# Optimization experiments

Hardware: AMD Instinct MI355X
Metric: run time of the kernel (lower is better)

The kernel has to match this reference:

```python
import jax, jax.numpy as jnp
import numpy as np

WS = 8      # window size
NH = 8      # num heads
ED = 256    # embed dim
HD = ED // NH  # head dim


def conv2d(x, w, b):
    # x: [B,C,H,W], w: [O,I,3,3] (torch OIHW), SAME padding, stride 1
    y = jax.lax.conv_general_dilated(x, w, (1, 1), 'SAME',
                                     dimension_numbers=('NCHW', 'OIHW', 'NCHW'))
    return y + b[None, :, None, None]


def linear(x, w, b):
    # torch Linear: y = x @ W^T + b, w: [out,in]
    return jnp.einsum('bnc,oc->bno', x, w) + b


def window_partition(x, ws):
    B, C, H, W = x.shape
    x = x.reshape(B, C, H // ws, ws, W // ws, ws)
    x = jnp.transpose(x, (0, 2, 4, 3, 5, 1))  # B, H/ws, W/ws, ws, ws, C
    return x.reshape(-1, ws * ws, C)


def window_reverse(win, H, W, ws, C):
    nW = (H // ws) * (W // ws)
    B = win.shape[0] // nW
    x = win.reshape(B, H // ws, W // ws, ws, ws, C)
    x = jnp.transpose(x, (0, 5, 1, 3, 2, 4))
    return x.reshape(B, C, H, W)


def setup_inputs() -> dict:
    key = jax.random.key(0)
    ks = jax.random.split(key, 24)
    s = 0.02
    inp = {
        'xmap': jax.random.normal(ks[0], (4, ED, 256, 256), jnp.float32),
        'xfeat': jax.random.normal(ks[1], (4, 32, 256, 256), jnp.float32),
        'cmap_w': jax.random.normal(ks[2], (ED, ED, 3, 3), jnp.float32) * s,
        'cmap_b': jnp.zeros((ED,), jnp.float32),
        'cfeat_w': jax.random.normal(ks[3], (ED, 32, 3, 3), jnp.float32) * s,
        'cfeat_b': jnp.zeros((ED,), jnp.float32),
        'qxmap_w': jax.random.normal(ks[4], (ED, ED), jnp.float32) * s,
        'qxmap_b': jnp.zeros((ED,), jnp.float32),
        'kxmap_w': jax.random.normal(ks[5], (ED, ED), jnp.float32) * s,
        'kxmap_b': jnp.zeros((ED,), jnp.float32),
        'vxmap_w': jax.random.normal(ks[6], (ED, ED), jnp.float32) * s,
        'vxmap_b': jnp.zeros((ED,), jnp.float32),
        'qxfeat_w': jax.random.normal(ks[7], (ED, ED), jnp.float32) * s,
        'qxfeat_b': jnp.zeros((ED,), jnp.float32),
        'kxfeat_w': jax.random.normal(ks[8], (ED, ED), jnp.float32) * s,
        'kxfeat_b': jnp.zeros((ED,), jnp.float32),
        'proj_w': jax.random.normal(ks[9], (ED, ED), jnp.float32) * s,
        'proj_b': jnp.zeros((ED,), jnp.float32),
        'cout_w': jax.random.normal(ks[10], (ED, ED, 3, 3), jnp.float32) * s,
        'cout_b': jnp.zeros((ED,), jnp.float32),
    }
    return inp


def reference(xmap, xfeat, cmap_w, cmap_b, cfeat_w, cfeat_b,
              qxmap_w, qxmap_b, kxmap_w, kxmap_b, vxmap_w, vxmap_b,
              qxfeat_w, qxfeat_b, kxfeat_w, kxfeat_b,
              proj_w, proj_b, cout_w, cout_b):
    B, C, H, W = xmap.shape  # xfeat matches spatial size -> no interpolate branch
    xmap = conv2d(xmap, cmap_w, cmap_b)
    identity = xmap
    wm = window_partition(xmap, WS)                        # [Bw, N, C]
    wf = window_partition(conv2d(xfeat, cfeat_w, cfeat_b), WS)
    Bw, N, _ = wm.shape

    def heads(t):
        return jnp.transpose(t.reshape(Bw, N, NH, HD), (0, 2, 1, 3))  # [Bw,H,N,D]

    q_m = heads(linear(wm, qxmap_w, qxmap_b))
    k_m = heads(linear(wm, kxmap_w, kxmap_b))
    v_m = heads(linear(wm, vxmap_w, vxmap_b))
    q_f = heads(linear(wf, qxfeat_w, qxfeat_b))
    k_f = heads(linear(wf, kxfeat_w, kxfeat_b))

    q_g = jax.nn.sigmoid(q_f) * q_m
    k_g = jax.nn.sigmoid(k_f) * k_m

    scale = 1.0 / jnp.sqrt(jnp.asarray(HD, q_g.dtype))
    attn = jax.nn.softmax(jnp.einsum('bhnd,bhmd->bhnm', q_g, k_g) * scale, axis=-1)
    out = jnp.einsum('bhnm,bhmd->bhnd', attn, v_m)         # [Bw,H,N,D]
    out = jnp.transpose(out, (0, 2, 1, 3)).reshape(Bw, N, C)
    out = window_reverse(linear(out, proj_w, proj_b), H, W, WS, C)
    return conv2d(out, cout_w, cout_b) + identity
```

## Files before the change

### kernel.cpp

```cpp
#include <hip/hip_runtime.h>
#include <hip/hip_bf16.h>
#include <cstdint>
#include <math.h>

using bf16 = __hip_bfloat16;
typedef __attribute__((ext_vector_type(4))) float f32x4;
typedef __attribute__((ext_vector_type(8))) short s16x8;
typedef __attribute__((ext_vector_type(4))) short s16x4;

#define AS3(p) ((__attribute__((address_space(3))) void *)(p))
#define AS1(p) ((const __attribute__((address_space(1))) void *)(p))

static constexpr int Himg = 256, Wimg = 256, Bimg = 4;
static constexpr int HWimg = Himg * Wimg;
static constexpr int Ttok = Bimg * HWimg;

__device__ __forceinline__ void gld16(bf16* lds, const bf16* g) {
  __builtin_amdgcn_global_load_lds(AS1(g), AS3(lds), 16, 0, 0);
}

__device__ __forceinline__ unsigned short f2u(float f) {
  bf16 b = __float2bfloat16(f);
  unsigned short u; __builtin_memcpy(&u, &b, 2); return u;
}

__device__ __forceinline__ int remap_lin(int bid, int total) {
  return (bid & 7) * (total >> 3) + (bid >> 3);
}
__device__ __forceinline__ void remap_tile(int bid, int total, int NY, int BMv, int& t0, int& n0) {
  int lin = remap_lin(bid, total);
  t0 = (lin / NY) * BMv;
  n0 = (lin % NY) * 128;
}

__global__ void k_zero4k(float* p) {
  p[blockIdx.x * 256 + threadIdx.x] = 0.f;
}

__global__ void k_castf2b(const float* __restrict__ s, bf16* __restrict__ d, int n) {
  int i = blockIdx.x * 256 + threadIdx.x;
  if (i < n) d[i] = __float2bfloat16(s[i]);
}

__global__ void k_copyf(const float* __restrict__ s, float* __restrict__ d, int n) {
  int i = blockIdx.x * 256 + threadIdx.x;
  if (i < n) d[i] = s[i];
}

__global__ void k_permconv(const float* __restrict__ w, bf16* __restrict__ o, int I) {
  int idx = blockIdx.x * 256 + threadIdx.x;
  int tot = 256 * 9 * I;
  if (idx >= tot) return;
  int i   = idx % I;
  int rem = idx / I;
  int tap = rem % 9;
  int oc  = rem / 9;
  o[idx] = __float2bfloat16(w[(oc * I + i) * 9 + tap]);
}

__global__ void k_tohwc(const float* __restrict__ src, bf16* __restrict__ dst, int C) {
  int bh = blockIdx.x;
  int w0 = blockIdx.y * 32;
  int c0 = blockIdx.z * 32;
  int b = bh / Himg, h = bh % Himg;
  __shared__ float tile[32][33];
  int tid = threadIdx.x;
  int x = tid & 31, y = tid >> 5;
  const float* sp = src + (size_t)b * C * HWimg + (size_t)h * Wimg;
#pragma unroll
  for (int p = 0; p < 4; ++p) {
    int cl = y + p * 8;
    tile[cl][x] = sp[(size_t)(c0 + cl) * HWimg + w0 + x];
  }
  __syncthreads();
#pragma unroll
  for (int p = 0; p < 4; ++p) {
    int wl = y + p * 8;
    dst[((size_t)bh * Wimg + w0 + wl) * C + c0 + x] = __float2bfloat16(tile[x][wl]);
  }
}

template <int CIN, int TAPS, int EPI>
__global__ void __launch_bounds__(512, 1)
k_gemm8(const bf16* __restrict__ Ain, const bf16* __restrict__ BT,
        const float* __restrict__ bias,
        bf16* __restrict__ outb, int ldo, float* __restrict__ outf,
        const bf16* __restrict__ ident,
        const bf16* __restrict__ zp)
{
  constexpr int KTOT = TAPS * CIN;
  const int t0 = remap_lin(blockIdx.x, gridDim.x) * 256;
  const int tid  = threadIdx.x;
  const int wave = tid >> 6, lane = tid & 63;
  const int wr = wave >> 2, wc = wave & 3;
  const int fr = lane & 15, fq = lane >> 4;

  __shared__ __attribute__((aligned(16))) char arena[132608];
  bf16* A0k0 = (bf16*)(arena);
  bf16* A0k1 = (bf16*)(arena + 16384);
  bf16* A1k0 = (bf16*)(arena + 32768);
  bf16* A1k1 = (bf16*)(arena + 49152);
  bf16* B0k0 = (bf16*)(arena + 65536);
  bf16* B0k1 = (bf16*)(arena + 81920);
  bf16* B1k0 = (bf16*)(arena + 98304);
  bf16* B1k1 = (bf16*)(arena + 114688);

  f32x4 acc[8][4] = {};
  s16x8 bfr[4];

  const int slot8 = (fq ^ ((fr >> 1) & 3)) * 8;
  const int aoff  = (wr * 128 + fr) * 32 + slot8;
  const int boff  = (wc * 64 + fr) * 32 + slot8;
  const int ldsl  = (tid & 3) * 8;
  const int scol  = ((tid & 3) ^ ((tid >> 3) & 3)) * 8;
  const int srow  = tid >> 2;

  const bf16* Bb0 = BT + (size_t)srow * KTOT + scol;
  const bf16* Bb1 = BT + (size_t)(128 + srow) * KTOT + scol;
  const bf16* Aa0 = Ain + (size_t)(t0 + srow) * CIN + scol;
  const bf16* Aa1 = Ain + (size_t)(t0 + 128 + srow) * CIN + scol;
  const bf16 *a0c = Aa0, *a1c = Aa1, *a0n = Aa0, *a1n = Aa1;
  const int hU = (t0 >> 8) & 255;

  auto mkbase = [&](int tap, const bf16*& o0, const bf16*& o1) {
    const int dy = tap / 3 - 1, dx = tap % 3 - 1;
    const bool rowok = ((unsigned)(hU + dy)) < 256u;
    const long gb = (long)t0 + dy * Wimg + dx;
    o0 = (rowok && (unsigned)(srow + dx) < 256u)
             ? Ain + (gb + srow) * CIN + scol : zp + scol;
    o1 = (rowok && (unsigned)(128 + srow + dx) < 256u)
             ? Ain + (gb + 128 + srow) * CIN + scol : zp + scol;
  };

#define STA8(DST, P0, P1, CE) do {                                              \
    gld16(DST + srow * 32 + ldsl, (P0) + (CE));                                 \
    gld16(DST + (128 + srow) * 32 + ldsl, (P1) + (CE));                         \
  } while (0)
#define STB8(DST, KE) do {                                                      \
    gld16(DST + srow * 32 + ldsl, Bb0 + (KE));                                  \
    gld16(DST + (128 + srow) * 32 + ldsl, Bb1 + (KE));                          \
  } while (0)

#define NVMs
#define VM4 asm volatile("s_waitcnt vmcnt(4)" ::: "memory")
#define VM0 asm volatile("s_waitcnt vmcnt(0)" ::: "memory")

#define PHO(RA, RB, MH, READB, ...) do {                                         \
    s16x8 af_[4];                                                                \
    _Pragma("unroll") for (int q_ = 0; q_ < 4; ++q_)                             \
      af_[q_] = *(const s16x8*)((RA) + aoff + ((MH) * 4 + q_) * 512);            \
    if (READB) {                                                                 \
      _Pragma("unroll") for (int n_ = 0; n_ < 4; ++n_)                           \
        bfr[n_] = *(const s16x8*)((RB) + boff + n_ * 512);                       \
    }                                                                            \
    __VA_ARGS__;                                                                 \
    asm volatile("s_waitcnt lgkmcnt(0)" ::: "memory");                           \
    __builtin_amdgcn_sched_barrier(0);                                           \
    __builtin_amdgcn_s_setprio(1);                                               \
    _Pragma("unroll") for (int q_ = 0; q_ < 4; ++q_)                             \
      _Pragma("unroll") for (int n_ = 0; n_ < 4; ++n_)                           \
        acc[(MH) * 4 + q_][n_] = __builtin_amdgcn_mfma_f32_16x16x32_bf16(        \
            af_[q_], bfr[n_], acc[(MH) * 4 + q_][n_], 0, 0, 0);                  \
    __builtin_amdgcn_s_setprio(0);                                               \
  } while (0)

#define PHE(RA, RB, MH, READB, VMSTMT, ...) do {                                 \
    s16x8 af_[4];                                                                \
    _Pragma("unroll") for (int q_ = 0; q_ < 4; ++q_)                             \
      af_[q_] = *(const s16x8*)((RA) + aoff + ((MH) * 4 + q_) * 512);            \
    if (READB) {                                                                 \
      _Pragma("unroll") for (int n_ = 0; n_ < 4; ++n_)                           \
        bfr[n_] = *(const s16x8*)((RB) + boff + n_ * 512);                       \
    }                                                                            \
    __VA_ARGS__;                                                                 \
    VMSTMT;                                                                      \
    __builtin_amdgcn_sched_barrier(0);                                           \
    __builtin_amdgcn_s_barrier();                                                \
    asm volatile("s_waitcnt lgkmcnt(0)" ::: "memory");                           \
    __builtin_amdgcn_sched_barrier(0);                                           \
    __builtin_amdgcn_s_setprio(1);                                               \
    _Pragma("unroll") for (int q_ = 0; q_ < 4; ++q_)                             \
      _Pragma("unroll") for (int n_ = 0; n_ < 4; ++n_)                           \
        acc[(MH) * 4 + q_][n_] = __builtin_amdgcn_mfma_f32_16x16x32_bf16(        \
            af_[q_], bfr[n_], acc[(MH) * 4 + q_][n_], 0, 0, 0);                  \
    __builtin_amdgcn_s_setprio(0);                                               \
  } while (0)

  if constexpr (TAPS == 9 && CIN == 256) {
    mkbase(0, a0c, a1c);
    mkbase(1, a0n, a1n);
    STA8(A0k0, a0c, a1c, 0);  STB8(B0k0, 0);
    STA8(A0k1, a0c, a1c, 32); STB8(B0k1, 32);
    VM4;
    __builtin_amdgcn_s_barrier();
#pragma unroll 1
    for (int tap = 0; tap < 8; ++tap) {
      PHO(A0k0, B0k0, 0, 1, STA8(A1k0, a0c, a1c, 64));
      PHE(A0k0, B0k0, 1, 0, VM4, STB8(B1k0, 64));
      PHO(A0k1, B0k1, 0, 1, STA8(A1k1, a0c, a1c, 96));
      PHE(A0k1, B0k1, 1, 0, VM4, STB8(B1k1, 96));
      PHO(A1k0, B1k0, 0, 1, STA8(A0k0, a0c, a1c, 128));
      PHE(A1k0, B1k0, 1, 0, VM4, STB8(B0k0, 128));
      PHO(A1k1, B1k1, 0, 1, STA8(A0k1, a0c, a1c, 160));
      PHE(A1k1, B1k1, 1, 0, VM4, STB8(B0k1, 160));
      PHO(A0k0, B0k0, 0, 1, STA8(A1k0, a0c, a1c, 192));
      PHE(A0k0, B0k0, 1, 0, VM4, STB8(B1k0, 192));
      PHO(A0k1, B0k1, 0, 1, STA8(A1k1, a0c, a1c, 224));
      PHE(A0k1, B0k1, 1, 0, VM4, STB8(B1k1, 224));
      PHO(A1k0, B1k0, 0, 1, STA8(A0k0, a0n, a1n, 0));
      PHE(A1k0, B1k0, 1, 0, VM4, STB8(B0k0, 256));
      PHO(A1k1, B1k1, 0, 1, STA8(A0k1, a0n, a1n, 32));
      PHE(A1k1, B1k1, 1, 0, VM4, STB8(B0k1, 288));
      a0c = a0n; a1c = a1n;
      if (tap + 2 < 9) mkbase(tap + 2, a0n, a1n);
      Bb0 += 256; Bb1 += 256;
    }
    PHO(A0k0, B0k0, 0, 1, STA8(A1k0, a0c, a1c, 64));
    PHE(A0k0, B0k0, 1, 0, VM4, STB8(B1k0, 64));
    PHO(A0k1, B0k1, 0, 1, STA8(A1k1, a0c, a1c, 96));
    PHE(A0k1, B0k1, 1, 0, VM4, STB8(B1k1, 96));
    PHO(A1k0, B1k0, 0, 1, STA8(A0k0, a0c, a1c, 128));
    PHE(A1k0, B1k0, 1, 0, VM4, STB8(B0k0, 128));
    PHO(A1k1, B1k1, 0, 1, STA8(A0k1, a0c, a1c, 160));
    PHE(A1k1, B1k1, 1, 0, VM4, STB8(B0k1, 160));
    PHO(A0k0, B0k0, 0, 1, STA8(A1k0, a0c, a1c, 192));
    PHE(A0k0, B0k0, 1, 0, VM4, STB8(B1k0, 192));
    PHO(A0k1, B0k1, 0, 1, STA8(A1k1, a0c, a1c, 224));
    PHE(A0k1, B0k1, 1, 0, VM4, STB8(B1k1, 224));
    PHO(A1k0, B1k0, 0, 1, );
    PHE(A1k0, B1k0, 1, 0, VM0, );
    PHO(A1k1, B1k1, 0, 1, );
    PHE(A1k1, B1k1, 1, 0, NVMs, );
  } else if constexpr (TAPS == 9) {
    mkbase(0, a0c, a1c);
    STA8(A0k0, a0c, a1c, 0);  STB8(B0k0, 0);
    mkbase(1, a0c, a1c);
    STA8(A0k1, a0c, a1c, 0);  STB8(B0k1, 32);
    VM4;
    __builtin_amdgcn_s_barrier();
    PHO(A0k0, B0k0, 0, 1, mkbase(2, a0c, a1c); STA8(A1k0, a0c, a1c, 0));
    PHE(A0k0, B0k0, 1, 0, VM4, STB8(B1k0, 64));
    PHO(A0k1, B0k1, 0, 1, mkbase(3, a0c, a1c); STA8(A1k1, a0c, a1c, 0));
    PHE(A0k1, B0k1, 1, 0, VM4, STB8(B1k1, 96));
    PHO(A1k0, B1k0, 0, 1, mkbase(4, a0c, a1c); STA8(A0k0, a0c, a1c, 0));
    PHE(A1k0, B1k0, 1, 0, VM4, STB8(B0k0, 128));
    PHO(A1k1, B1k1, 0, 1, mkbase(5, a0c, a1c); STA8(A0k1, a0c, a1c, 0));
    PHE(A1k1, B1k1, 1, 0, VM4, STB8(B0k1, 160));
    PHO(A0k0, B0k0, 0, 1, mkbase(6, a0c, a1c); STA8(A1k0, a0c, a1c, 0));
    PHE(A0k0, B0k0, 1, 0, VM4, STB8(B1k0, 192));
    PHO(A0k1, B0k1, 0, 1, mkbase(7, a0c, a1c); STA8(A1k1, a0c, a1c, 0));
    PHE(A0k1, B0k1, 1, 0, VM4, STB8(B1k1, 224));
    PHO(A1k0, B1k0, 0, 1, mkbase(8, a0c, a1c); STA8(A0k0, a0c, a1c, 0));
    PHE(A1k0, B1k0, 1, 0, VM4, STB8(B0k0, 256));
    PHO(A1k1, B1k1, 0, 1, );
    PHE(A1k1, B1k1, 1, 0, VM0, );
    PHO(A0k0, B0k0, 0, 1, );
    PHE(A0k0, B0k0, 1, 0, NVMs, );
  } else {
    STA8(A0k0, Aa0, Aa1, 0);  STB8(B0k0, 0);
    STA8(A0k1, Aa0, Aa1, 32); STB8(B0k1, 32);
    VM4;
    __builtin_amdgcn_s_barrier();
    PHO(A0k0, B0k0, 0, 1, STA8(A1k0, Aa0, Aa1, 64));
    PHE(A0k0, B0k0, 1, 0, VM4, STB8(B1k0, 64));
    PHO(A0k1, B0k1, 0, 1, STA8(A1k1, Aa0, Aa1, 96));
    PHE(A0k1, B0k1, 1, 0, VM4, STB8(B1k1, 96));
    PHO(A1k0, B1k0, 0, 1, STA8(A0k0, Aa0, Aa1, 128));
    PHE(A1k0, B1k0, 1, 0, VM4, STB8(B0k0, 128));
    PHO(A1k1, B1k1, 0, 1, STA8(A0k1, Aa0, Aa1, 160));
    PHE(A1k1, B1k1, 1, 0, VM4, STB8(B0k1, 160));
    PHO(A0k0, B0k0, 0, 1, STA8(A1k0, Aa0, Aa1, 192));
    PHE(A0k0, B0k0, 1, 0, VM4, STB8(B1k0, 192));
    PHO(A0k1, B0k1, 0, 1, STA8(A1k1, Aa0, Aa1, 224));
    PHE(A0k1, B0k1, 1, 0, VM4, STB8(B1k1, 224));
    PHO(A1k0, B1k0, 0, 1, );
    PHE(A1k0, B1k0, 1, 0, VM0, );
    PHO(A1k1, B1k1, 0, 1, );
    PHE(A1k1, B1k1, 1, 0, NVMs, );
  }
#undef PHO
#undef PHE
#undef STA8
#undef STB8
#undef NVMs
#undef VM4
#undef VM0

  if (EPI == 2) {
    float* TR = (float*)arena;
    const int bN = t0 >> 16, hN = (t0 >> 8) & 255;
#pragma unroll 1
    for (int chunk = 0; chunk < 2; ++chunk) {
      __builtin_amdgcn_s_barrier();
      if ((wc >> 1) == chunk) {
#pragma unroll
        for (int m = 0; m < 8; ++m)
#pragma unroll
          for (int n = 0; n < 4; ++n) {
            const int col = wc * 64 + n * 16 + fr;
            const int cl  = (wc & 1) * 64 + n * 16 + fr;
            const float bb = bias[col];
#pragma unroll
            for (int j = 0; j < 4; ++j) {
              const int row = wr * 128 + m * 16 + fq * 4 + j;
              const size_t t = (size_t)t0 + row;
              TR[cl * 259 + row] = acc[m][n][j] + bb +
                                   __bfloat162float(ident[t * 256 + col]);
            }
          }
      }
      __builtin_amdgcn_s_barrier();
      {
        const int cl = tid >> 2, wo = (tid & 3) * 4;
        const int c = chunk * 128 + cl;
        float* dp = outf + (((size_t)bN * 256 + c) * 256 + hN) * 256;
#pragma unroll
        for (int q = 0; q < 16; ++q)
          *(f32x4*)(dp + wo + q * 16) = *(const f32x4*)&TR[cl * 259 + wo + q * 16];
      }
    }
    return;
  }

#pragma unroll
  for (int m = 0; m < 8; ++m) {
#pragma unroll
    for (int n = 0; n < 4; ++n) {
      const int col = wc * 64 + n * 16 + fr;
#pragma unroll
      for (int j = 0; j < 4; ++j) {
        const int row = wr * 128 + m * 16 + fq * 4 + j;
        const size_t t = (size_t)t0 + row;
        outb[t * ldo + col] = __float2bfloat16(acc[m][n][j] + bias[col]);
      }
    }
  }
}

__global__ void __launch_bounds__(256, 2)
k_gemm_qkv(const bf16* __restrict__ Am, const bf16* __restrict__ Af,
           const bf16* __restrict__ Bm, const bf16* __restrict__ Bf,
           const float* __restrict__ bm, const float* __restrict__ bfi,
           bf16* __restrict__ out)
{
  int t0, n0;
  remap_tile(blockIdx.x, gridDim.x, 4, 128, t0, n0);
  const int tid = threadIdx.x;
  const int wave = tid >> 6, lane = tid & 63;
  const int seg = lane & 3;
  const int rr  = lane >> 2;

  __shared__ bf16 sA0[128 * 32];
  __shared__ bf16 sA1[128 * 32];
  __shared__ bf16 sA2[128 * 32];
  __shared__ bf16 sB0[128 * 32];
  __shared__ bf16 sB1[128 * 32];
  __shared__ bf16 sB2[128 * 32];

  f32x4 accm[4][4] = {};
  f32x4 accf[4][4] = {};

  const int wr = wave >> 1, wc = wave & 1;
  const int fr = lane & 15, fq = lane >> 4;
  const int sseg = (seg ^ ((rr >> 1) & 3)) * 8;
  const int slot = (fq ^ ((fr >> 1) & 3)) * 8;

#define STAGEQ(WA, WB, SV) do {                                                 \
    const int k0_ = ((SV) >> 1) * 32;                                           \
    const bf16* A_ = ((SV) & 1) ? Af : Am;                                      \
    const bf16* B_ = ((SV) & 1) ? Bf : Bm;                                      \
    _Pragma("unroll") for (int i_ = 0; i_ < 2; ++i_) {                          \
      const int r_ = wave * 32 + i_ * 16 + rr;                                  \
      gld16(WA + (wave * 32 + i_ * 16) * 32, A_ + (size_t)(t0 + r_) * 256 + k0_ + sseg); \
      gld16(WB + (wave * 32 + i_ * 16) * 32, B_ + (size_t)(n0 + r_) * 256 + k0_ + sseg); \
    }                                                                           \
  } while (0)

#define QSTEP(RA, RB, WA, WB, SV, LASTF) do {                                   \
    if (LASTF) { asm volatile("s_waitcnt vmcnt(0)" ::: "memory"); }             \
    else       { asm volatile("s_waitcnt vmcnt(4)" ::: "memory"); }             \
    __builtin_amdgcn_s_barrier();                                               \
    s16x8 af_[4], bf_[4];                                                       \
    _Pragma("unroll") for (int m_ = 0; m_ < 4; ++m_)                            \
      af_[m_] = *(const s16x8*)(RA + (wr * 64 + m_ * 16 + fr) * 32 + slot);     \
    _Pragma("unroll") for (int n_ = 0; n_ < 4; ++n_)                            \
      bf_[n_] = *(const s16x8*)(RB + (wc * 64 + n_ * 16 + fr) * 32 + slot);     \
    if ((SV) + 2 < 16) STAGEQ(WA, WB, (SV) + 2);                                \
    __builtin_amdgcn_s_setprio(1);                                              \
    if ((SV) & 1) {                                                             \
      _Pragma("unroll") for (int m_ = 0; m_ < 4; ++m_)                          \
        _Pragma("unroll") for (int n_ = 0; n_ < 4; ++n_)                        \
          accf[m_][n_] = __builtin_amdgcn_mfma_f32_16x16x32_bf16(af_[m_], bf_[n_], accf[m_][n_], 0, 0, 0); \
    } else {                                                                    \
      _Pragma("unroll") for (int m_ = 0; m_ < 4; ++m_)                          \
        _Pragma("unroll") for (int n_ = 0; n_ < 4; ++n_)                        \
          accm[m_][n_] = __builtin_amdgcn_mfma_f32_16x16x32_bf16(af_[m_], bf_[n_], accm[m_][n_], 0, 0, 0); \
    }                                                                           \
    __builtin_amdgcn_s_setprio(0);                                              \
  } while (0)

  STAGEQ(sA0, sB0, 0);
  STAGEQ(sA1, sB1, 1);

  int s = 0;
#pragma unroll 1
  for (; s < 15; s += 3) {
    QSTEP(sA0, sB0, sA2, sB2, s,     false);
    QSTEP(sA1, sB1, sA0, sB0, s + 1, false);
    QSTEP(sA2, sB2, sA1, sB1, s + 2, false);
  }
  QSTEP(sA0, sB0, sA2, sB2, 15, true);
#undef QSTEP
#undef STAGEQ

#pragma unroll
  for (int m = 0; m < 4; ++m) {
#pragma unroll
    for (int n = 0; n < 4; ++n) {
      const int col = n0 + wc * 64 + n * 16 + fr;
#pragma unroll
      for (int j = 0; j < 4; ++j) {
        const int row = wr * 64 + m * 16 + fq * 4 + j;
        const size_t t = (size_t)t0 + row;
        float v = accm[m][n][j] + bm[col];
        const float g = accf[m][n][j] + bfi[col];
        v *= 1.f / (1.f + __expf(-g));
        out[t * 768 + col] = __float2bfloat16(v);
      }
    }
  }
}

__global__ void __launch_bounds__(256, 4)
k_attn_mfma(const bf16* __restrict__ qkv, bf16* __restrict__ out) {
  __shared__ short smem[4 * 7424];
  const int tid = threadIdx.x;
  const int wave = tid >> 6, lane = tid & 63;
  const int fr = lane & 15, fq = lane >> 4;
  const int wi = blockIdx.x >> 1;
  const int head = (blockIdx.x & 1) * 4 + wave;
  const int b = wi >> 10, rem = wi & 1023, wh = rem >> 5, ww = rem & 31;
  const size_t tbase = (size_t)b * HWimg + (size_t)(wh * 8) * Wimg + ww * 8;

  short* Qs = smem + wave * 7424;
  short* Ks = Qs + 2560;
  short* VT = Qs + 5120;
  short* P  = Qs;
  short* Ol = Qs;

  auto tok = [&](int i) -> size_t {
    return tbase + (size_t)(i >> 3) * Wimg + (i & 7);
  };

  {
    const bf16* tb = qkv + tok(lane) * 768 + head * 32;
#pragma unroll
    for (int c = 0; c < 4; ++c) {
      s16x8 qv = *(const s16x8*)(tb + c * 8);
      s16x8 kv = *(const s16x8*)(tb + 256 + c * 8);
      s16x8 vv = *(const s16x8*)(tb + 512 + c * 8);
      *(s16x8*)(Qs + lane * 40 + c * 8) = qv;
      *(s16x8*)(Ks + lane * 40 + c * 8) = kv;
#pragma unroll
      for (int e = 0; e < 8; ++e) VT[(c * 8 + e) * 72 + lane] = vv[e];
    }
  }

  s16x8 kf[4], qf[4];
#pragma unroll
  for (int m = 0; m < 4; ++m)
    kf[m] = *(const s16x8*)(Ks + (fr + 16 * m) * 40 + fq * 8);
#pragma unroll
  for (int n = 0; n < 4; ++n)
    qf[n] = *(const s16x8*)(Qs + (fr + 16 * n) * 40 + fq * 8);

  f32x4 st[4][4] = {};
#pragma unroll
  for (int m = 0; m < 4; ++m)
#pragma unroll
    for (int n = 0; n < 4; ++n)
      st[m][n] = __builtin_amdgcn_mfma_f32_16x16x32_bf16(kf[m], qf[n], st[m][n], 0, 0, 0);

  const float scale = 0.17677669529663688f;
  float invs[4];
#pragma unroll
  for (int n = 0; n < 4; ++n) {
    float mx = -1e30f;
#pragma unroll
    for (int m = 0; m < 4; ++m)
#pragma unroll
      for (int j = 0; j < 4; ++j) mx = fmaxf(mx, st[m][n][j]);
    mx = fmaxf(mx, __shfl_xor(mx, 16));
    mx = fmaxf(mx, __shfl_xor(mx, 32));
    float sum = 0.f;
#pragma unroll
    for (int m = 0; m < 4; ++m) {
      s16x4 pk;
#pragma unroll
      for (int j = 0; j < 4; ++j) {
        float e = __expf((st[m][n][j] - mx) * scale);
        sum += e;
        pk[j] = (short)f2u(e);
      }
      *(s16x4*)(P + (fr + 16 * n) * 72 + 16 * m + 4 * fq) = pk;
    }
    sum += __shfl_xor(sum, 16);
    sum += __shfl_xor(sum, 32);
    invs[n] = 1.f / sum;
  }

  f32x4 oc[4][2] = {};
#pragma unroll
  for (int ks = 0; ks < 2; ++ks) {
    s16x8 pf[4], vf[2];
#pragma unroll
    for (int m = 0; m < 4; ++m)
      pf[m] = *(const s16x8*)(P + (fr + 16 * m) * 72 + ks * 32 + fq * 8);
#pragma unroll
    for (int n = 0; n < 2; ++n)
      vf[n] = *(const s16x8*)(VT + (fr + 16 * n) * 72 + ks * 32 + fq * 8);
#pragma unroll
    for (int m = 0; m < 4; ++m)
#pragma unroll
      for (int n = 0; n < 2; ++n)
        oc[m][n] = __builtin_amdgcn_mfma_f32_16x16x32_bf16(pf[m], vf[n], oc[m][n], 0, 0, 0);
  }

#pragma unroll
  for (int m = 0; m < 4; ++m)
#pragma unroll
    for (int j = 0; j < 4; ++j) {
      const float inv = __shfl(invs[m], 4 * fq + j);
      const int q = 16 * m + 4 * fq + j;
#pragma unroll
      for (int n = 0; n < 2; ++n)
        Ol[q * 40 + fr + 16 * n] = (short)f2u(oc[m][n][j] * inv);
    }
  {
    bf16* op = out + tok(lane) * 256 + head * 32;
#pragma unroll
    for (int c = 0; c < 4; ++c)
      *(s16x8*)(op + c * 8) = *(const s16x8*)(Ol + lane * 40 + c * 8);
  }
}

extern "C" void kernel_launch(void* const* d_in, const int* in_sizes, int n_in,
                              void* d_out, int out_size, void* d_ws, size_t ws_size,
                              hipStream_t stream) {
  const float* xmap    = (const float*)d_in[0];
  const float* xfeat   = (const float*)d_in[1];
  const float* cmap_w  = (const float*)d_in[2];
  const float* cmap_b  = (const float*)d_in[3];
  const float* cfeat_w = (const float*)d_in[4];
  const float* cfeat_b = (const float*)d_in[5];
  const float* qxmap_w = (const float*)d_in[6];
  const float* qxmap_b = (const float*)d_in[7];
  const float* kxmap_w = (const float*)d_in[8];
  const float* kxmap_b = (const float*)d_in[9];
  const float* vxmap_w = (const float*)d_in[10];
  const float* vxmap_b = (const float*)d_in[11];
  const float* qxfeat_w = (const float*)d_in[12];
  const float* qxfeat_b = (const float*)d_in[13];
  const float* kxfeat_w = (const float*)d_in[14];
  const float* kxfeat_b = (const float*)d_in[15];
  const float* proj_w  = (const float*)d_in[16];
  const float* proj_b  = (const float*)d_in[17];
  const float* cout_w  = (const float*)d_in[18];
  const float* cout_b  = (const float*)d_in[19];

  uint8_t* ws = (uint8_t*)d_ws;
  size_t off = 0;
  auto alloc = [&](size_t bytes) -> void* {
    void* p = ws + off;
    off += (bytes + 255) & ~(size_t)255;
    return p;
  };
  float* zp       = (float*)alloc(4096);
  bf16* cmap_wT   = (bf16*)alloc((size_t)2304 * 256 * 2);
  bf16* cout_wT   = (bf16*)alloc((size_t)2304 * 256 * 2);
  bf16* cfeat_wT  = (bf16*)alloc((size_t)288 * 256 * 2);
  bf16* lin_qkv_wT= (bf16*)alloc((size_t)768 * 256 * 2);
  bf16* lin_f_wT  = (bf16*)alloc((size_t)512 * 256 * 2);
  bf16* proj_wT   = (bf16*)alloc((size_t)256 * 256 * 2);
  float* bias_qkv = (float*)alloc(768 * 4);
  float* bias_f   = (float*)alloc(512 * 4);
  bf16* xm_nhwc   = (bf16*)alloc((size_t)Ttok * 256 * 2);
  bf16* xf_nhwc   = (bf16*)alloc((size_t)Ttok * 32 * 2);
  bf16* xc        = (bf16*)alloc((size_t)Ttok * 256 * 2);
  bf16* fc        = (bf16*)alloc((size_t)Ttok * 256 * 2);
  bf16* qkv       = (bf16*)alloc((size_t)Ttok * 768 * 2);
  bf16* attn_out  = xm_nhwc;
  bf16* proj_out  = fc;
  bf16* zpb = (bf16*)zp;

  k_zero4k<<<4, 256, 0, stream>>>(zp);
  k_permconv<<<(256 * 9 * 256 + 255) / 256, 256, 0, stream>>>(cmap_w, cmap_wT, 256);
  k_permconv<<<(256 * 9 * 256 + 255) / 256, 256, 0, stream>>>(cout_w, cout_wT, 256);
  k_permconv<<<(256 * 9 * 32 + 255) / 256, 256, 0, stream>>>(cfeat_w, cfeat_wT, 32);
  k_castf2b<<<256, 256, 0, stream>>>(qxmap_w, lin_qkv_wT, 65536);
  k_castf2b<<<256, 256, 0, stream>>>(kxmap_w, lin_qkv_wT + 65536, 65536);
  k_castf2b<<<256, 256, 0, stream>>>(vxmap_w, lin_qkv_wT + 131072, 65536);
  k_castf2b<<<256, 256, 0, stream>>>(qxfeat_w, lin_f_wT, 65536);
  k_castf2b<<<256, 256, 0, stream>>>(kxfeat_w, lin_f_wT + 65536, 65536);
  k_castf2b<<<256, 256, 0, stream>>>(proj_w, proj_wT, 65536);
  k_copyf<<<1, 256, 0, stream>>>(qxmap_b, bias_qkv, 256);
  k_copyf<<<1, 256, 0, stream>>>(kxmap_b, bias_qkv + 256, 256);
  k_copyf<<<1, 256, 0, stream>>>(vxmap_b, bias_qkv + 512, 256);
  k_copyf<<<1, 256, 0, stream>>>(qxfeat_b, bias_f, 256);
  k_copyf<<<1, 256, 0, stream>>>(kxfeat_b, bias_f + 256, 256);

  k_tohwc<<<dim3(Bimg * Himg, Wimg / 32, 256 / 32), 256, 0, stream>>>(xmap, xm_nhwc, 256);
  k_tohwc<<<dim3(Bimg * Himg, Wimg / 32, 1), 256, 0, stream>>>(xfeat, xf_nhwc, 32);

  const int NB = Ttok / 256;
  k_gemm8<256, 9, 0><<<dim3(NB), dim3(512), 0, stream>>>(
      xm_nhwc, cmap_wT, cmap_b, xc, 256, nullptr, nullptr, zpb);
  k_gemm8<32, 9, 0><<<dim3(NB), dim3(512), 0, stream>>>(
      xf_nhwc, cfeat_wT, cfeat_b, fc, 256, nullptr, nullptr, zpb);
  k_gemm8<256, 1, 0><<<dim3(NB), dim3(512), 0, stream>>>(
      xc, lin_qkv_wT + 131072, bias_qkv + 512, qkv + 512, 768, nullptr, nullptr, zpb);
  k_gemm_qkv<<<dim3((Ttok / 128) * 4), dim3(256), 0, stream>>>(
      xc, fc, lin_qkv_wT, lin_f_wT, bias_qkv, bias_f, qkv);
  k_attn_mfma<<<dim3(4096 * 2), dim3(256), 0, stream>>>(qkv, attn_out);
  k_gemm8<256, 1, 0><<<dim3(NB), dim3(512), 0, stream>>>(
      attn_out, proj_wT, proj_b, proj_out, 256, nullptr, nullptr, zpb);
  k_gemm8<256, 9, 2><<<dim3(NB), dim3(512), 0, stream>>>(
      proj_out, cout_wT, cout_b, nullptr, 0, (float*)d_out, xc, zpb);
}
```

Before: 1.392 ms.

## Restructure QKV gated GEMM into four-buffer half-step pipelined schedule

Replaces the three-buffer LDS ring in the fused QKV/gate GEMM with a four-buffer ring and a fully unrolled schedule. Each K-step is split into two half-phases, and A and B global-to-LDS loads are interleaved between the MFMA halves, with explicit lgkmcnt waits and sched_barriers. The aim is to overlap global loads with MFMA work more finely and to cut the number of block barriers per step. The cost is extra LDS (which may lower occupancy at two blocks per CU) and a hand-tuned ordering of vmcnt waits and barriers that must be exactly right to stay correct.

```diff
diff --git a/kernel.cpp b/kernel.cpp
--- a/kernel.cpp
+++ b/kernel.cpp
@@ -353,65 +353,116 @@
   __shared__ bf16 sA0[128 * 32];
   __shared__ bf16 sA1[128 * 32];
   __shared__ bf16 sA2[128 * 32];
+  __shared__ bf16 sA3[128 * 32];
   __shared__ bf16 sB0[128 * 32];
   __shared__ bf16 sB1[128 * 32];
   __shared__ bf16 sB2[128 * 32];
+  __shared__ bf16 sB3[128 * 32];
 
   f32x4 accm[4][4] = {};
   f32x4 accf[4][4] = {};
+  s16x8 bfr[4];
 
   const int wr = wave >> 1, wc = wave & 1;
   const int fr = lane & 15, fq = lane >> 4;
   const int sseg = (seg ^ ((rr >> 1) & 3)) * 8;
   const int slot = (fq ^ ((fr >> 1) & 3)) * 8;
 
-#define STAGEQ(WA, WB, SV) do {                                                 \
-    const int k0_ = ((SV) >> 1) * 32;                                           \
-    const bf16* A_ = ((SV) & 1) ? Af : Am;                                      \
-    const bf16* B_ = ((SV) & 1) ? Bf : Bm;                                      \
-    _Pragma("unroll") for (int i_ = 0; i_ < 2; ++i_) {                          \
-      const int r_ = wave * 32 + i_ * 16 + rr;                                  \
-      gld16(WA + (wave * 32 + i_ * 16) * 32, A_ + (size_t)(t0 + r_) * 256 + k0_ + sseg); \
-      gld16(WB + (wave * 32 + i_ * 16) * 32, B_ + (size_t)(n0 + r_) * 256 + k0_ + sseg); \
-    }                                                                           \
-  } while (0)
-
-#define QSTEP(RA, RB, WA, WB, SV, LASTF) do {                                   \
-    if (LASTF) { asm volatile("s_waitcnt vmcnt(0)" ::: "memory"); }             \
-    else       { asm volatile("s_waitcnt vmcnt(4)" ::: "memory"); }             \
+#define STQA(DST, AP, K0) do {                                                  \
+    _Pragma("unroll") for (int i_ = 0; i_ < 2; ++i_)                            \
+      gld16(DST + (wave * 32 + i_ * 16) * 32,                                   \
+            (AP) + (size_t)(t0 + wave * 32 + i_ * 16 + rr) * 256 + (K0) + sseg);\
+  } while (0)
+#define STQB(DST, BP, K0) do {                                                  \
+    _Pragma("unroll") for (int i_ = 0; i_ < 2; ++i_)                            \
+      gld16(DST + (wave * 32 + i_ * 16) * 32,                                   \
+            (BP) + (size_t)(n0 + wave * 32 + i_ * 16 + rr) * 256 + (K0) + sseg);\
+  } while (0)
+
+#define NVMs
+#define VM4 asm volatile("s_waitcnt vmcnt(4)" ::: "memory")
+#define VM0 asm volatile("s_waitcnt vmcnt(0)" ::: "memory")
+
+#define PHOQ(RA, RB, ACC, ...) do {                                             \
+    s16x8 af_[2];                                                               \
+    _Pragma("unroll") for (int m_ = 0; m_ < 2; ++m_)                            \
+      af_[m_] = *(const s16x8*)((RA) + (wr * 64 + m_ * 16 + fr) * 32 + slot);   \
+    _Pragma("unroll") for (int n_ = 0; n_ < 4; ++n_)                            \
+      bfr[n_] = *(const s16x8*)((RB) + (wc * 64 + n_ * 16 + fr) * 32 + slot);   \
+    __VA_ARGS__;                                                                \
+    asm volatile("s_waitcnt lgkmcnt(0)" ::: "memory");                          \
+    __builtin_amdgcn_sched_barrier(0);                                          \
+    __builtin_amdgcn_s_setprio(1);                                              \
+    _Pragma("unroll") for (int m_ = 0; m_ < 2; ++m_)                            \
+      _Pragma("unroll") for (int n_ = 0; n_ < 4; ++n_)                          \
+        ACC[m_][n_] = __builtin_amdgcn_mfma_f32_16x16x32_bf16(                  \
+            af_[m_], bfr[n_], ACC[m_][n_], 0, 0, 0);                            \
+    __builtin_amdgcn_s_setprio(0);                                              \
+  } while (0)
+
+#define PHEQ(RA, ACC, VMSTMT, ...) do {                                         \
+    s16x8 af_[2];                                                               \
+    _Pragma("unroll") for (int m_ = 0; m_ < 2; ++m_)                            \
+      af_[m_] = *(const s16x8*)((RA) + (wr * 64 + (2 + m_) * 16 + fr) * 32 + slot); \
+    __VA_ARGS__;                                                                \
+    VMSTMT;                                                                     \
+    __builtin_amdgcn_sched_barrier(0);                                          \
     __builtin_amdgcn_s_barrier();                                               \
-    s16x8 af_[4], bf_[4];                                                       \
-    _Pragma("unroll") for (int m_ = 0; m_ < 4; ++m_)                            \
-      af_[m_] = *(const s16x8*)(RA + (wr * 64 + m_ * 16 + fr) * 32 + slot);     \
-    _Pragma("unroll") for (int n_ = 0; n_ < 4; ++n_)                            \
-      bf_[n_] = *(const s16x8*)(RB + (wc * 64 + n_ * 16 + fr) * 32 + slot);     \
-    if ((SV) + 2 < 16) STAGEQ(WA, WB, (SV) + 2);                                \
+    asm volatile("s_waitcnt lgkmcnt(0)" ::: "memory");                          \
+    __builtin_amdgcn_sched_barrier(0);                                          \
     __builtin_amdgcn_s_setprio(1);                                              \
-    if ((SV) & 1) {                                                             \
-      _Pragma("unroll") for (int m_ = 0; m_ < 4; ++m_)                          \
-        _Pragma("unroll") for (int n_ = 0; n_ < 4; ++n_)                        \
-          accf[m_][n_] = __builtin_amdgcn_mfma_f32_16x16x32_bf16(af_[m_], bf_[n_], accf[m_][n_], 0, 0, 0); \
-    } else {                                                                    \
-      _Pragma("unroll") for (int m_ = 0; m_ < 4; ++m_)                          \
-        _Pragma("unroll") for (int n_ = 0; n_ < 4; ++n_)                        \
-          accm[m_][n_] = __builtin_amdgcn_mfma_f32_16x16x32_bf16(af_[m_], bf_[n_], accm[m_][n_], 0, 0, 0); \
-    }                                                                           \
+    _Pragma("unroll") for (int m_ = 0; m_ < 2; ++m_)                            \
+      _Pragma("unroll") for (int n_ = 0; n_ < 4; ++n_)                          \
+        ACC[2 + m_][n_] = __builtin_amdgcn_mfma_f32_16x16x32_bf16(              \
+            af_[m_], bfr[n_], ACC[2 + m_][n_], 0, 0, 0);                        \
     __builtin_amdgcn_s_setprio(0);                                              \
   } while (0)
 
-  STAGEQ(sA0, sB0, 0);
-  STAGEQ(sA1, sB1, 1);
-
-  int s = 0;
-#pragma unroll 1
-  for (; s < 15; s += 3) {
-    QSTEP(sA0, sB0, sA2, sB2, s,     false);
-    QSTEP(sA1, sB1, sA0, sB0, s + 1, false);
-    QSTEP(sA2, sB2, sA1, sB1, s + 2, false);
-  }
-  QSTEP(sA0, sB0, sA2, sB2, 15, true);
-#undef QSTEP
-#undef STAGEQ
+  STQA(sA0, Am, 0);  STQB(sB0, Bm, 0);
+  STQA(sA1, Af, 0);  STQB(sB1, Bf, 0);
+  VM4;
+  __builtin_amdgcn_s_barrier();
+
+  PHOQ(sA0, sB0, accm, STQA(sA2, Am, 32));
+  PHEQ(sA0, accm, VM4, STQB(sB2, Bm, 32));
+  PHOQ(sA1, sB1, accf, STQA(sA3, Af, 32));
+  PHEQ(sA1, accf, VM4, STQB(sB3, Bf, 32));
+  PHOQ(sA2, sB2, accm, STQA(sA0, Am, 64));
+  PHEQ(sA2, accm, VM4, STQB(sB0, Bm, 64));
+  PHOQ(sA3, sB3, accf, STQA(sA1, Af, 64));
+  PHEQ(sA3, accf, VM4, STQB(sB1, Bf, 64));
+  PHOQ(sA0, sB0, accm, STQA(sA2, Am, 96));
+  PHEQ(sA0, accm, VM4, STQB(sB2, Bm, 96));
+  PHOQ(sA1, sB1, accf, STQA(sA3, Af, 96));
+  PHEQ(sA1, accf, VM4, STQB(sB3, Bf, 96));
+  PHOQ(sA2, sB2, accm, STQA(sA0, Am, 128));
+  PHEQ(sA2, accm, VM4, STQB(sB0, Bm, 128));
+  PHOQ(sA3, sB3, accf, STQA(sA1, Af, 128));
+  PHEQ(sA3, accf, VM4, STQB(sB1, Bf, 128));
+  PHOQ(sA0, sB0, accm, STQA(sA2, Am, 160));
+  PHEQ(sA0, accm, VM4, STQB(sB2, Bm, 160));
+  PHOQ(sA1, sB1, accf, STQA(sA3, Af, 160));
+  PHEQ(sA1, accf, VM4, STQB(sB3, Bf, 160));
+  PHOQ(sA2, sB2, accm, STQA(sA0, Am, 192));
+  PHEQ(sA2, accm, VM4, STQB(sB0, Bm, 192));
+  PHOQ(sA3, sB3, accf, STQA(sA1, Af, 192));
+  PHEQ(sA3, accf, VM4, STQB(sB1, Bf, 192));
+  PHOQ(sA0, sB0, accm, STQA(sA2, Am, 224));
+  PHEQ(sA0, accm, VM4, STQB(sB2, Bm, 224));
+  PHOQ(sA1, sB1, accf, STQA(sA3, Af, 224));
+  PHEQ(sA1, accf, VM4, STQB(sB3, Bf, 224));
+  PHOQ(sA2, sB2, accm, );
+  PHEQ(sA2, accm, VM0, );
+  PHOQ(sA3, sB3, accf, );
+  PHEQ(sA3, accf, NVMs, );
+
+#undef PHOQ
+#undef PHEQ
+#undef STQA
+#undef STQB
+#undef NVMs
+#undef VM4
+#undef VM0
 
 #pragma unroll
   for (int m = 0; m < 4; ++m) {
```

Result: no change. 1.386 ms (-0.4%).
